# Kernel optimization log

Measured on AMD Instinct MI355X. Metric: run time of the kernel, lower is better.

## Reference

```python
import jax, jax.numpy as jnp
import numpy as np

EMBED = 768
HEADS = 12
FFN = 3072
EPS = 1e-5

def _linear_params(key, din, dout):
    k1, k2 = jax.random.split(key)
    s = 1.0 / np.sqrt(din)
    W = jax.random.uniform(k1, (din, dout), minval=-s, maxval=s, dtype=jnp.float32)
    b = jax.random.uniform(k2, (dout,), minval=-s, maxval=s, dtype=jnp.float32)
    return W, b

def setup_inputs() -> dict:
    key = jax.random.key(0)
    ks = jax.random.split(key, 8)
    x = jax.random.normal(ks[0], (1, 4096, EMBED), dtype=jnp.float32)
    Wq, bq = _linear_params(ks[1], EMBED, EMBED)
    Wk, bk = _linear_params(ks[2], EMBED, EMBED)
    Wv, bv = _linear_params(ks[3], EMBED, EMBED)
    Wo, bo = _linear_params(ks[4], EMBED, EMBED)
    W1, b1 = _linear_params(ks[5], EMBED, FFN)
    W2, b2 = _linear_params(ks[6], FFN, EMBED)
    ln1_g = jnp.ones((EMBED,), jnp.float32); ln1_b = jnp.zeros((EMBED,), jnp.float32)
    ln2_g = jnp.ones((EMBED,), jnp.float32); ln2_b = jnp.zeros((EMBED,), jnp.float32)
    return {"x": x, "Wq": Wq, "bq": bq, "Wk": Wk, "bk": bk, "Wv": Wv, "bv": bv,
            "Wo": Wo, "bo": bo, "ln1_g": ln1_g, "ln1_b": ln1_b,
            "ln2_g": ln2_g, "ln2_b": ln2_b, "W1": W1, "b1": b1, "W2": W2, "b2": b2}

def _layernorm(x, g, b):
    mu = jnp.mean(x, axis=-1, keepdims=True)
    var = jnp.mean(jnp.square(x - mu), axis=-1, keepdims=True)
    return (x - mu) * jax.lax.rsqrt(var + EPS) * g + b

def _block(x, Wq, bq, Wk, bk, Wv, bv, Wo, bo, ln1_g, ln1_b, ln2_g, ln2_b, W1, b1, W2, b2):
    B, T, C = x.shape
    H = HEADS
    D = C // H
    # pre-LN
    h = _layernorm(x, ln1_g, ln1_b)
    # naive causal self-attention with explicit [B,H,T,T] scores (as in source)
    q = (h @ Wq + bq).reshape(B, T, H, D).transpose(0, 2, 1, 3)  # bhtd
    k = (h @ Wk + bk).reshape(B, T, H, D).transpose(0, 2, 1, 3)
    v = (h @ Wv + bv).reshape(B, T, H, D).transpose(0, 2, 1, 3)
    scores = jnp.einsum('bhqd,bhkd->bhqk', q, k) / jnp.sqrt(jnp.float32(D))
    causal = jnp.tril(jnp.ones((T, T), dtype=bool))  # True = keep
    scores = jnp.where(causal, scores, -jnp.inf)
    attn = jax.nn.softmax(scores, axis=-1)
    ctx = jnp.einsum('bhqk,bhkd->bhqd', attn, v)
    ctx = ctx.transpose(0, 2, 1, 3).reshape(B, T, C)
    y = ctx @ Wo + bo
    x = y + h  # residual onto ln1 output (source adds to post-LN x)
    # second LN + MLP
    h2 = _layernorm(x, ln2_g, ln2_b)
    m = jax.nn.gelu(h2 @ W1 + b1, approximate=False) @ W2 + b2
    return m + h2

def reference(x, Wq, bq, Wk, bk, Wv, bv, Wo, bo, ln1_g, ln1_b, ln2_g, ln2_b, W1, b1, W2, b2):
    return _block(x, Wq, bq, Wk, bk, Wv, bv, Wo, bo, ln1_g, ln1_b, ln2_g, ln2_b, W1, b1, W2, b2)
```

## Files before the change

### kernel.cpp

```cpp
#include <hip/hip_runtime.h>
#include <math.h>

#define EMBED 768
#define FFN_D 3072
#define TSEQ 4096
#define NHEAD 12
#define DHEAD 64
#define CQKV 2304
#define NSPLIT 4
#define NQITEMS 192
#define SC2Q 0.180336880111120419f

typedef _Float16 f16;
typedef __attribute__((ext_vector_type(2))) _Float16 f16x2;
typedef __attribute__((ext_vector_type(4))) _Float16 f16x4;
typedef __attribute__((ext_vector_type(8))) _Float16 f16x8;
typedef __attribute__((ext_vector_type(4))) float f32x4;

#if __has_builtin(__builtin_amdgcn_exp2f)
#define EXP2(x) __builtin_amdgcn_exp2f(x)
#else
#define EXP2(x) exp2f(x)
#endif

__device__ __forceinline__ f16x2 pkrtz(float a, float b) {
    return __builtin_bit_cast(f16x2, __builtin_amdgcn_cvt_pkrtz(a, b));
}

__device__ __forceinline__ void gload16(const f16* g, f16* lds) {
    __builtin_amdgcn_global_load_lds((const __attribute__((address_space(1))) void*)g,
                                     (__attribute__((address_space(3))) void*)lds, 16, 0, 0);
}

__global__ __launch_bounds__(256) void prep_kernel(const float* __restrict__ Wq,
                                                   const float* __restrict__ Wk,
                                                   const float* __restrict__ Wv,
                                                   const float* __restrict__ Wo,
                                                   const float* __restrict__ W1,
                                                   const float* __restrict__ W2,
                                                   const float* __restrict__ bq,
                                                   const float* __restrict__ bk,
                                                   const float* __restrict__ bv,
                                                   f16* __restrict__ WqkvT,
                                                   f16* __restrict__ WoT,
                                                   f16* __restrict__ W1T,
                                                   f16* __restrict__ W2T,
                                                   float* __restrict__ bqkv) {
    const int b = blockIdx.x;
    const int t = threadIdx.x;
    if (b == 1728) {
#pragma unroll
        for (int i = 0; i < 9; i++) {
            int idx = i * 256 + t;
            if (idx < 768) bqkv[idx] = bq[idx];
            else if (idx < 1536) bqkv[idx] = bk[idx - 768];
            else if (idx < 2304) bqkv[idx] = bv[idx - 1536];
        }
        return;
    }
    const float* W; f16* WT; int din, dout, local;
    if (b < 144)       { W = Wq; WT = WqkvT;                 din = 768;  dout = 768;  local = b; }
    else if (b < 288)  { W = Wk; WT = WqkvT + 768 * 768;     din = 768;  dout = 768;  local = b - 144; }
    else if (b < 432)  { W = Wv; WT = WqkvT + 2 * 768 * 768; din = 768;  dout = 768;  local = b - 288; }
    else if (b < 576)  { W = Wo; WT = WoT;                   din = 768;  dout = 768;  local = b - 432; }
    else if (b < 1152) { W = W1; WT = W1T;                   din = 768;  dout = 3072; local = b - 576; }
    else               { W = W2; WT = W2T;                   din = 3072; dout = 768;  local = b - 1152; }
    const int ntx = dout / 64;
    const int j0 = (local % ntx) * 64;
    const int i0 = (local / ntx) * 64;
    __shared__ float tile[64][65];
    const int tx = t & 63;
    const int ty = t >> 6;
#pragma unroll
    for (int rr = ty; rr < 64; rr += 4)
        tile[rr][tx] = W[(size_t)(i0 + rr) * dout + j0 + tx];
    __syncthreads();
    const int half = t & 31;
    const int rw = t >> 5;
#pragma unroll
    for (int rr = rw; rr < 64; rr += 8) {
        f16x2 v = {(f16)tile[2 * half][rr], (f16)tile[2 * half + 1][rr]};
        *(f16x2*)&WT[(size_t)(j0 + rr) * din + i0 + 2 * half] = v;
    }
}

__global__ __launch_bounds__(256) void ln_kernel(const float* __restrict__ x,
                                                 const float* __restrict__ g,
                                                 const float* __restrict__ b,
                                                 f16* __restrict__ hh) {
    const int row = blockIdx.x;
    const float* xr = x + (size_t)row * EMBED;
    const int t = threadIdx.x;
    float v0 = xr[t], v1 = xr[t + 256], v2 = xr[t + 512];
    float s = v0 + v1 + v2;
#pragma unroll
    for (int m = 1; m < 64; m <<= 1) s += __shfl_xor(s, m);
    __shared__ float red[4], red2[4];
    const int wid = t >> 6, lane = t & 63;
    if (lane == 0) red[wid] = s;
    __syncthreads();
    float mean = (red[0] + red[1] + red[2] + red[3]) * (1.0f / 768.0f);
    float d0 = v0 - mean, d1 = v1 - mean, d2 = v2 - mean;
    float ss = d0 * d0 + d1 * d1 + d2 * d2;
#pragma unroll
    for (int m = 1; m < 64; m <<= 1) ss += __shfl_xor(ss, m);
    if (lane == 0) red2[wid] = ss;
    __syncthreads();
    float inv = rsqrtf((red2[0] + red2[1] + red2[2] + red2[3]) * (1.0f / 768.0f) + 1e-5f);
    size_t base = (size_t)row * EMBED;
    hh[base + t]       = (f16)(d0 * inv * g[t] + b[t]);
    hh[base + t + 256] = (f16)(d1 * inv * g[t + 256] + b[t + 256]);
    hh[base + t + 512] = (f16)(d2 * inv * g[t + 512] + b[t + 512]);
}

template <int EPI, int BM, int BN>
__global__ __launch_bounds__(256) void gemm_kernel(const f16* __restrict__ A,
                                                   const f16* __restrict__ BT,
                                                   const float* __restrict__ bias,
                                                   const f16* __restrict__ resh,
                                                   float* __restrict__ outf,
                                                   f16* __restrict__ outh,
                                                   f16* __restrict__ vtout,
                                                   int M, int N, int K) {
    constexpr int IM = BM / 32;
    constexpr int JN = BN / 32;
    __shared__ __align__(16) f16 As[BM][64];
    __shared__ __align__(16) f16 Bs[BN][64];
    const int t = threadIdx.x;
    const int nbx = gridDim.x;
    const int nwg = nbx * gridDim.y;
    int bid = blockIdx.x + blockIdx.y * nbx;
    bid = (bid & 7) * (nwg >> 3) + (bid >> 3);
    const int m0 = (bid / nbx) * BM;
    const int n0 = (bid % nbx) * BN;
    const int wid = t >> 6;
    const int lane = t & 63;
    const int wm = (wid >> 1) * (BM / 2);
    const int wn = (wid & 1) * (BN / 2);
    const int lr = lane & 15;
    const int quad = lane >> 4;
    const int sr = lane >> 3;
    const int scn = (lane & 7) ^ sr;
    const int xv = lr & 7;

    f32x4 zero = {0.f, 0.f, 0.f, 0.f};
    f32x4 acc[IM][JN];
#pragma unroll
    for (int i = 0; i < IM; i++)
#pragma unroll
        for (int j = 0; j < JN; j++) acc[i][j] = zero;

    const f16* Ap = A + (size_t)(m0 + wid * (BM / 4) + sr) * K + scn * 8;
    const f16* Bp = BT + (size_t)(n0 + wid * (BN / 4) + sr) * K + scn * 8;

    for (int k0 = 0; k0 < K; k0 += 64) {
        __syncthreads();
#pragma unroll
        for (int c = 0; c < BM / 32; c++)
            gload16(Ap + (size_t)(c * 8) * K + k0, &As[wid * (BM / 4) + c * 8][0]);
#pragma unroll
        for (int c = 0; c < BN / 32; c++)
            gload16(Bp + (size_t)(c * 8) * K + k0, &Bs[wid * (BN / 4) + c * 8][0]);
        __syncthreads();
#pragma unroll
        for (int ks = 0; ks < 2; ks++) {
            f16x8 af[IM], bf[JN];
#pragma unroll
            for (int i = 0; i < IM; i++)
                af[i] = *(const f16x8*)&As[wm + i * 16 + lr][((ks * 4 + quad) ^ xv) * 8];
#pragma unroll
            for (int j = 0; j < JN; j++)
                bf[j] = *(const f16x8*)&Bs[wn + j * 16 + lr][((ks * 4 + quad) ^ xv) * 8];
#pragma unroll
            for (int i = 0; i < IM; i++)
#pragma unroll
                for (int j = 0; j < JN; j++)
                    acc[i][j] = __builtin_amdgcn_mfma_f32_16x16x32_f16(bf[j], af[i], acc[i][j], 0, 0, 0);
        }
    }

    const bool vsec = (EPI == 0) && (n0 >= 2 * EMBED);
#pragma unroll
    for (int i = 0; i < IM; i++) {
        const int row = m0 + wm + i * 16 + lr;
#pragma unroll
        for (int j = 0; j < JN; j++) {
            const int col = n0 + wn + j * 16 + quad * 4;
            const float4 bv = *(const float4*)&bias[col];
            float v0 = acc[i][j][0] + bv.x;
            float v1 = acc[i][j][1] + bv.y;
            float v2 = acc[i][j][2] + bv.z;
            float v3 = acc[i][j][3] + bv.w;
            const size_t idx = (size_t)row * N + col;
            if (EPI == 0) {
                if (vsec) {
                    const int c0 = col - 2 * EMBED;
                    vtout[(size_t)(c0 + 0) * TSEQ + row] = (f16)v0;
                    vtout[(size_t)(c0 + 1) * TSEQ + row] = (f16)v1;
                    vtout[(size_t)(c0 + 2) * TSEQ + row] = (f16)v2;
                    vtout[(size_t)(c0 + 3) * TSEQ + row] = (f16)v3;
                } else {
                    const float qs = (col < EMBED) ? SC2Q : 1.0f;
                    f16x4 hv = {(f16)(v0 * qs), (f16)(v1 * qs), (f16)(v2 * qs), (f16)(v3 * qs)};
                    *(f16x4*)&outh[idx] = hv;
                }
            } else if (EPI == 1) {
                const f16x4 rr = *(const f16x4*)&resh[idx];
                f32x4 ov = {v0 + (float)rr[0], v1 + (float)rr[1], v2 + (float)rr[2], v3 + (float)rr[3]};
                *(f32x4*)&outf[idx] = ov;
            } else {
                f16x4 hv = {(f16)(0.5f * v0 * (1.0f + erff(v0 * 0.70710678118654752f))),
                            (f16)(0.5f * v1 * (1.0f + erff(v1 * 0.70710678118654752f))),
                            (f16)(0.5f * v2 * (1.0f + erff(v2 * 0.70710678118654752f))),
                            (f16)(0.5f * v3 * (1.0f + erff(v3 * 0.70710678118654752f)))};
                *(f16x4*)&outh[idx] = hv;
            }
        }
    }
}

__global__ __launch_bounds__(256) void attn_kernel(const f16* __restrict__ qkv,
                                                   const f16* __restrict__ vT,
                                                   f16* __restrict__ OpartH,
                                                   float2* __restrict__ ml,
                                                   int* __restrict__ ctr) {
    __shared__ __align__(16) f16 Ks[64][72];
    __shared__ __align__(16) f16 Vt[64][72];
    __shared__ int s_item;
    const int t = threadIdx.x;
    const int wid = t >> 6;
    const int lane = t & 63;
    const int lr = lane & 15;
    const int quad = lane >> 4;
    const int srow = t >> 3;
    const int scol = (t & 7) * 8;
    const int pA = (t & 1) * 16 + ((t >> 1) & 1) * 4 + (t & 4) * 8;
    const int xq = blockIdx.x & 7;

    for (;;) {
        __syncthreads();
        if (t == 0) s_item = atomicAdd(&ctr[xq], 1);
        __syncthreads();
        const int item = s_item;
        if (item >= NQITEMS) return;
        const int qb = 31 - item / 6;
        const int u = xq * 6 + item % 6;
        const int h = u >> 2;
        const int sp = u & 3;
        const int q0 = qb * 128;

        const int nkb = 2 * qb + 2;
        const int chunk = (nkb + NSPLIT - 1) / NSPLIT;
        const int kb0 = sp * chunk;
        const int kb1 = min(nkb, kb0 + chunk);
        const int wrow0 = q0 + wid * 32;

        float m_i[2] = {-INFINITY, -INFINITY};
        float l_lane[2] = {0.f, 0.f};
        f32x4 zero = {0.f, 0.f, 0.f, 0.f};
        f32x4 o[4][2];
#pragma unroll
        for (int dt = 0; dt < 4; dt++)
#pragma unroll
            for (int qt = 0; qt < 2; qt++) o[dt][qt] = zero;

        f16x8 qf[2][2];
        int4 kreg[2], vreg[2];
        const f16* kbase = qkv + EMBED + (size_t)h * DHEAD;
        const f16* vbase = vT + (size_t)h * DHEAD * TSEQ;
        if (kb0 < kb1) {
#pragma unroll
            for (int qt = 0; qt < 2; qt++)
#pragma unroll
                for (int dh = 0; dh < 2; dh++)
                    qf[qt][dh] = *(const f16x8*)(qkv + (size_t)(wrow0 + qt * 16 + lr) * CQKV
                                                 + h * DHEAD + dh * 32 + quad * 8);
            const int k0 = kb0 * 64;
#pragma unroll
            for (int p = 0; p < 2; p++) {
                kreg[p] = *(const int4*)(kbase + (size_t)(k0 + p * 32 + srow) * CQKV + scol);
                vreg[p] = *(const int4*)(vbase + (size_t)(p * 32 + srow) * TSEQ + k0 + scol);
            }
        }

        for (int kb = kb0; kb < kb1; ++kb) {
            const int k0 = kb * 64;
            __syncthreads();
#pragma unroll
            for (int p = 0; p < 2; p++) {
                *(int4*)&Ks[p * 32 + srow][scol] = kreg[p];
                *(int2*)&Vt[p * 32 + srow][pA]     = make_int2(vreg[p].x, vreg[p].y);
                *(int2*)&Vt[p * 32 + srow][pA + 8] = make_int2(vreg[p].z, vreg[p].w);
            }
            __syncthreads();
            if (kb + 1 < kb1) {
                const int kn = (kb + 1) * 64;
#pragma unroll
                for (int p = 0; p < 2; p++) {
                    kreg[p] = *(const int4*)(kbase + (size_t)(kn + p * 32 + srow) * CQKV + scol);
                    vreg[p] = *(const int4*)(vbase + (size_t)(p * 32 + srow) * TSEQ + kn + scol);
                }
            }

            if (k0 <= wrow0 + 31) {
                f32x4 s[4][2];
#pragma unroll
                for (int kt = 0; kt < 4; kt++)
#pragma unroll
                    for (int qt = 0; qt < 2; qt++) s[kt][qt] = zero;
#pragma unroll
                for (int dh = 0; dh < 2; dh++) {
#pragma unroll
                    for (int kt = 0; kt < 4; kt++) {
                        f16x8 kf = *(const f16x8*)&Ks[kt * 16 + lr][dh * 32 + quad * 8];
#pragma unroll
                        for (int qt = 0; qt < 2; qt++)
                            s[kt][qt] = __builtin_amdgcn_mfma_f32_16x16x32_f16(kf, qf[qt][dh], s[kt][qt], 0, 0, 0);
                    }
                }
                if (k0 + 63 > wrow0) {
#pragma unroll
                    for (int kt = 0; kt < 4; kt++)
#pragma unroll
                        for (int qt = 0; qt < 2; qt++)
#pragma unroll
                            for (int r = 0; r < 4; r++) {
                                int key = k0 + kt * 16 + quad * 4 + r;
                                int row = wrow0 + qt * 16 + lr;
                                if (key > row) s[kt][qt][r] = -INFINITY;
                            }
                }
                float mx[2];
#pragma unroll
                for (int qt = 0; qt < 2; qt++) {
                    float a[4];
#pragma unroll
                    for (int kt = 0; kt < 4; kt++)
                        a[kt] = fmaxf(fmaxf(s[kt][qt][0], s[kt][qt][1]),
                                      fmaxf(s[kt][qt][2], s[kt][qt][3]));
                    float m = fmaxf(fmaxf(a[0], a[1]), fmaxf(a[2], a[3]));
                    m = fmaxf(m, __shfl_xor(m, 16));
                    m = fmaxf(m, __shfl_xor(m, 32));
                    mx[qt] = m;
                }
                if (__any((mx[0] > m_i[0] + 4.f) || (mx[1] > m_i[1] + 4.f))) {
#pragma unroll
                    for (int qt = 0; qt < 2; qt++) {
                        float mn = fmaxf(m_i[qt], mx[qt]);
                        float al = EXP2(m_i[qt] - mn);
                        m_i[qt] = mn;
                        l_lane[qt] *= al;
#pragma unroll
                        for (int dt = 0; dt < 4; dt++)
#pragma unroll
                            for (int r = 0; r < 4; r++) o[dt][qt][r] *= al;
                    }
                }
                union PW { f16x8 v8; f16x2 h2[4]; };
                PW pw[2][2];
                float rs[2] = {0.f, 0.f};
#pragma unroll
                for (int kt = 0; kt < 4; kt++)
#pragma unroll
                    for (int qt = 0; qt < 2; qt++) {
                        float p0 = EXP2(s[kt][qt][0] - m_i[qt]);
                        float p1 = EXP2(s[kt][qt][1] - m_i[qt]);
                        float p2 = EXP2(s[kt][qt][2] - m_i[qt]);
                        float p3 = EXP2(s[kt][qt][3] - m_i[qt]);
                        rs[qt] += (p0 + p1) + (p2 + p3);
                        pw[kt >> 1][qt].h2[(kt & 1) * 2]     = pkrtz(p0, p1);
                        pw[kt >> 1][qt].h2[(kt & 1) * 2 + 1] = pkrtz(p2, p3);
                    }
#pragma unroll
                for (int qt = 0; qt < 2; qt++) l_lane[qt] += rs[qt];
#pragma unroll
                for (int s2 = 0; s2 < 2; s2++)
#pragma unroll
                    for (int dt = 0; dt < 4; dt++) {
                        f16x8 vf = *(const f16x8*)&Vt[dt * 16 + lr][s2 * 32 + quad * 8];
#pragma unroll
                        for (int qt = 0; qt < 2; qt++)
                            o[dt][qt] = __builtin_amdgcn_mfma_f32_16x16x32_f16(vf, pw[s2][qt].v8, o[dt][qt], 0, 0, 0);
                    }
            }
        }

        float l_i[2];
#pragma unroll
        for (int qt = 0; qt < 2; qt++) {
            float v2 = l_lane[qt];
            v2 += __shfl_xor(v2, 16);
            v2 += __shfl_xor(v2, 32);
            l_i[qt] = v2;
        }
        __syncthreads();
        f16* ob = ((wid & 2) ? &Vt[0][0] : &Ks[0][0]) + (wid & 1) * (32 * 72);
#pragma unroll
        for (int qt = 0; qt < 2; qt++)
#pragma unroll
            for (int dt = 0; dt < 4; dt++) {
                f16x4 oh = {(f16)o[dt][qt][0], (f16)o[dt][qt][1], (f16)o[dt][qt][2], (f16)o[dt][qt][3]};
                *(f16x4*)&ob[(qt * 16 + lr) * 72 + dt * 16 + quad * 4] = oh;
            }
        const int rl = lane >> 3;
        const int ck = lane & 7;
#pragma unroll
        for (int i = 0; i < 4; i++) {
            const int row_l = rl + i * 8;
            f16x8 val = *(const f16x8*)&ob[row_l * 72 + ck * 8];
            *(f16x8*)&OpartH[((size_t)sp * TSEQ + wrow0 + row_l) * EMBED + h * DHEAD + ck * 8] = val;
        }
#pragma unroll
        for (int qt = 0; qt < 2; qt++)
            if (quad == 0) {
                int row = wrow0 + qt * 16 + lr;
                ml[((size_t)sp * TSEQ + row) * NHEAD + h] = make_float2(m_i[qt], l_i[qt]);
            }
    }
}

__global__ __launch_bounds__(128) void attn_merge_kernel(const f16* __restrict__ OpartH,
                                                         const float2* __restrict__ ml,
                                                         f16* __restrict__ ctx) {
    const int row = blockIdx.x;
    const int t = threadIdx.x;
    __shared__ float wgt[NSPLIT][NHEAD];
    if (t < NHEAD) {
        float m[NSPLIT], l[NSPLIT];
        float M = -INFINITY;
#pragma unroll
        for (int s = 0; s < NSPLIT; s++) {
            float2 v = ml[((size_t)s * TSEQ + row) * NHEAD + t];
            m[s] = v.x; l[s] = v.y;
            M = fmaxf(M, m[s]);
        }
        float L = 0.f;
        float w[NSPLIT];
#pragma unroll
        for (int s = 0; s < NSPLIT; s++) {
            w[s] = exp2f(m[s] - M);
            L += l[s] * w[s];
        }
        float rL = 1.0f / L;
#pragma unroll
        for (int s = 0; s < NSPLIT; s++) wgt[s][t] = w[s] * rL;
    }
    __syncthreads();
    if (t < 96) {
        const int h = t >> 3;
        float acc[8] = {0.f, 0.f, 0.f, 0.f, 0.f, 0.f, 0.f, 0.f};
#pragma unroll
        for (int s = 0; s < NSPLIT; s++) {
            const float w = wgt[s][h];
            f16x8 v = *(const f16x8*)&OpartH[((size_t)s * TSEQ + row) * EMBED + t * 8];
#pragma unroll
            for (int e = 0; e < 8; e++) acc[e] += w * (float)v[e];
        }
        f16x8 out;
#pragma unroll
        for (int e = 0; e < 8; e++) out[e] = (f16)acc[e];
        *(f16x8*)&ctx[(size_t)row * EMBED + t * 8] = out;
    }
}

extern "C" void kernel_launch(void* const* d_in, const int* in_sizes, int n_in,
                              void* d_out, int out_size, void* d_ws, size_t ws_size,
                              hipStream_t stream) {
    const float* x     = (const float*)d_in[0];
    const float* Wq    = (const float*)d_in[1];
    const float* bq    = (const float*)d_in[2];
    const float* Wk    = (const float*)d_in[3];
    const float* bk    = (const float*)d_in[4];
    const float* Wv    = (const float*)d_in[5];
    const float* bv    = (const float*)d_in[6];
    const float* Wo    = (const float*)d_in[7];
    const float* bo    = (const float*)d_in[8];
    const float* ln1_g = (const float*)d_in[9];
    const float* ln1_b = (const float*)d_in[10];
    const float* ln2_g = (const float*)d_in[11];
    const float* ln2_b = (const float*)d_in[12];
    const float* W1    = (const float*)d_in[13];
    const float* b1    = (const float*)d_in[14];
    const float* W2    = (const float*)d_in[15];
    const float* b2    = (const float*)d_in[16];

    char* p = (char*)d_ws;
    auto alloc = [&](size_t bytes) -> void* {
        void* r = (void*)p;
        p += (bytes + 255) & ~(size_t)255;
        return r;
    };
    f16*   WqkvT = (f16*)alloc((size_t)CQKV * EMBED * 2);
    f16*   WoT   = (f16*)alloc((size_t)EMBED * EMBED * 2);
    f16*   W1T   = (f16*)alloc((size_t)FFN_D * EMBED * 2);
    f16*   W2T   = (f16*)alloc((size_t)EMBED * FFN_D * 2);
    float* bqkv  = (float*)alloc((size_t)CQKV * 4);
    f16*   hh    = (f16*)alloc((size_t)TSEQ * EMBED * 2);
    f16*   qkv   = (f16*)alloc((size_t)TSEQ * CQKV * 2);
    f16*   vT    = (f16*)alloc((size_t)EMBED * TSEQ * 2);
    f16*   ctx   = (f16*)alloc((size_t)TSEQ * EMBED * 2);
    float* x2    = (float*)alloc((size_t)TSEQ * EMBED * 4);
    f16*   h2h   = (f16*)alloc((size_t)TSEQ * EMBED * 2);
    f16*   m1    = (f16*)alloc((size_t)TSEQ * FFN_D * 2);
    int*   ctr   = (int*)alloc(256);

    f16*    OpartH = m1;
    float2* mlbuf  = (float2*)x2;

    dim3 blk(256);
    prep_kernel<<<dim3(1729), blk, 0, stream>>>(Wq, Wk, Wv, Wo, W1, W2, bq, bk, bv,
                                                WqkvT, WoT, W1T, W2T, bqkv);
    ln_kernel<<<dim3(TSEQ), blk, 0, stream>>>(x, ln1_g, ln1_b, hh);
    gemm_kernel<0, 64, 128><<<dim3(CQKV / 128, TSEQ / 64), blk, 0, stream>>>(
        hh, WqkvT, bqkv, nullptr, nullptr, qkv, vT, TSEQ, CQKV, EMBED);
    (void)hipMemsetAsync(ctr, 0, 256, stream);
    attn_kernel<<<dim3(768), blk, 0, stream>>>(qkv, vT, OpartH, mlbuf, ctr);
    attn_merge_kernel<<<dim3(TSEQ), dim3(128), 0, stream>>>(OpartH, mlbuf, ctx);
    gemm_kernel<1, 64, 64><<<dim3(EMBED / 64, TSEQ / 64), blk, 0, stream>>>(
        ctx, WoT, bo, hh, x2, nullptr, nullptr, TSEQ, EMBED, EMBED);
    ln_kernel<<<dim3(TSEQ), blk, 0, stream>>>(x2, ln2_g, ln2_b, h2h);
    gemm_kernel<2, 128, 128><<<dim3(FFN_D / 128, TSEQ / 128), blk, 0, stream>>>(
        h2h, W1T, b1, nullptr, nullptr, m1, nullptr, TSEQ, FFN_D, EMBED);
    gemm_kernel<1, 64, 64><<<dim3(EMBED / 64, TSEQ / 64), blk, 0, stream>>>(
        m1, W2T, b2, h2h, (float*)d_out, nullptr, nullptr, TSEQ, EMBED, FFN_D);
}
```

Baseline: 318.6 us.

## Double-buffer GEMM LDS tiles, batch merge rows, shrink FFN1 tile

The GEMM main loop now keeps two LDS buffers and issues the next K-tile's global-to-LDS copy before computing on the current one, dropping one barrier per iteration. The attention merge kernel handles four rows per block, with each thread computing its own split weights instead of going through shared memory and a barrier. The FFN1 GEMM moves from 128x128 to 64x128 tiles for more workgroups. Double buffering doubles LDS use, and its correctness depends on gload16 completing before the loop-end barrier.

```diff
diff --git a/kernel.cpp b/kernel.cpp
--- a/kernel.cpp
+++ b/kernel.cpp
@@ -124,8 +124,8 @@
                                                    int M, int N, int K) {
     constexpr int IM = BM / 32;
     constexpr int JN = BN / 32;
-    __shared__ __align__(16) f16 As[BM][64];
-    __shared__ __align__(16) f16 Bs[BN][64];
+    __shared__ __align__(16) f16 As[2][BM][64];
+    __shared__ __align__(16) f16 Bs[2][BN][64];
     const int t = threadIdx.x;
     const int nbx = gridDim.x;
     const int nwg = nbx * gridDim.y;
@@ -153,30 +153,37 @@
     const f16* Ap = A + (size_t)(m0 + wid * (BM / 4) + sr) * K + scn * 8;
     const f16* Bp = BT + (size_t)(n0 + wid * (BN / 4) + sr) * K + scn * 8;
 
+    auto stage = [&](int buf, int k0) {
+#pragma unroll
+        for (int c = 0; c < BM / 32; c++)
+            gload16(Ap + (size_t)(c * 8) * K + k0, &As[buf][wid * (BM / 4) + c * 8][0]);
+#pragma unroll
+        for (int c = 0; c < BN / 32; c++)
+            gload16(Bp + (size_t)(c * 8) * K + k0, &Bs[buf][wid * (BN / 4) + c * 8][0]);
+    };
+
+    stage(0, 0);
+    __syncthreads();
+    int cur = 0;
     for (int k0 = 0; k0 < K; k0 += 64) {
-        __syncthreads();
-#pragma unroll
-        for (int c = 0; c < BM / 32; c++)
-            gload16(Ap + (size_t)(c * 8) * K + k0, &As[wid * (BM / 4) + c * 8][0]);
-#pragma unroll
-        for (int c = 0; c < BN / 32; c++)
-            gload16(Bp + (size_t)(c * 8) * K + k0, &Bs[wid * (BN / 4) + c * 8][0]);
-        __syncthreads();
+        if (k0 + 64 < K) stage(cur ^ 1, k0 + 64);
 #pragma unroll
         for (int ks = 0; ks < 2; ks++) {
             f16x8 af[IM], bf[JN];
 #pragma unroll
             for (int i = 0; i < IM; i++)
-                af[i] = *(const f16x8*)&As[wm + i * 16 + lr][((ks * 4 + quad) ^ xv) * 8];
+                af[i] = *(const f16x8*)&As[cur][wm + i * 16 + lr][((ks * 4 + quad) ^ xv) * 8];
 #pragma unroll
             for (int j = 0; j < JN; j++)
-                bf[j] = *(const f16x8*)&Bs[wn + j * 16 + lr][((ks * 4 + quad) ^ xv) * 8];
+                bf[j] = *(const f16x8*)&Bs[cur][wn + j * 16 + lr][((ks * 4 + quad) ^ xv) * 8];
 #pragma unroll
             for (int i = 0; i < IM; i++)
 #pragma unroll
                 for (int j = 0; j < JN; j++)
                     acc[i][j] = __builtin_amdgcn_mfma_f32_16x16x32_f16(bf[j], af[i], acc[i][j], 0, 0, 0);
         }
+        __syncthreads();
+        cur ^= 1;
     }
 
     const bool vsec = (EPI == 0) && (n0 >= 2 * EMBED);
@@ -422,15 +429,17 @@
 __global__ __launch_bounds__(128) void attn_merge_kernel(const f16* __restrict__ OpartH,
                                                          const float2* __restrict__ ml,
                                                          f16* __restrict__ ctx) {
-    const int row = blockIdx.x;
     const int t = threadIdx.x;
-    __shared__ float wgt[NSPLIT][NHEAD];
-    if (t < NHEAD) {
+    if (t >= 96) return;
+    const int h = t >> 3;
+#pragma unroll
+    for (int r = 0; r < 4; r++) {
+        const int row = blockIdx.x * 4 + r;
         float m[NSPLIT], l[NSPLIT];
         float M = -INFINITY;
 #pragma unroll
         for (int s = 0; s < NSPLIT; s++) {
-            float2 v = ml[((size_t)s * TSEQ + row) * NHEAD + t];
+            float2 v = ml[((size_t)s * TSEQ + row) * NHEAD + h];
             m[s] = v.x; l[s] = v.y;
             M = fmaxf(M, m[s]);
         }
@@ -441,20 +450,14 @@
             w[s] = exp2f(m[s] - M);
             L += l[s] * w[s];
         }
-        float rL = 1.0f / L;
-#pragma unroll
-        for (int s = 0; s < NSPLIT; s++) wgt[s][t] = w[s] * rL;
-    }
-    __syncthreads();
-    if (t < 96) {
-        const int h = t >> 3;
+        const float rL = 1.0f / L;
         float acc[8] = {0.f, 0.f, 0.f, 0.f, 0.f, 0.f, 0.f, 0.f};
 #pragma unroll
         for (int s = 0; s < NSPLIT; s++) {
-            const float w = wgt[s][h];
+            const float ws = w[s] * rL;
             f16x8 v = *(const f16x8*)&OpartH[((size_t)s * TSEQ + row) * EMBED + t * 8];
 #pragma unroll
-            for (int e = 0; e < 8; e++) acc[e] += w * (float)v[e];
+            for (int e = 0; e < 8; e++) acc[e] += ws * (float)v[e];
         }
         f16x8 out;
 #pragma unroll
@@ -515,11 +518,11 @@
         hh, WqkvT, bqkv, nullptr, nullptr, qkv, vT, TSEQ, CQKV, EMBED);
     (void)hipMemsetAsync(ctr, 0, 256, stream);
     attn_kernel<<<dim3(768), blk, 0, stream>>>(qkv, vT, OpartH, mlbuf, ctr);
-    attn_merge_kernel<<<dim3(TSEQ), dim3(128), 0, stream>>>(OpartH, mlbuf, ctx);
+    attn_merge_kernel<<<dim3(TSEQ / 4), dim3(128), 0, stream>>>(OpartH, mlbuf, ctx);
     gemm_kernel<1, 64, 64><<<dim3(EMBED / 64, TSEQ / 64), blk, 0, stream>>>(
         ctx, WoT, bo, hh, x2, nullptr, nullptr, TSEQ, EMBED, EMBED);
     ln_kernel<<<dim3(TSEQ), blk, 0, stream>>>(x2, ln2_g, ln2_b, h2h);
-    gemm_kernel<2, 128, 128><<<dim3(FFN_D / 128, TSEQ / 128), blk, 0, stream>>>(
+    gemm_kernel<2, 64, 128><<<dim3(FFN_D / 128, TSEQ / 64), blk, 0, stream>>>(
         h2h, W1T, b1, nullptr, nullptr, m1, nullptr, TSEQ, FFN_D, EMBED);
     gemm_kernel<1, 64, 64><<<dim3(EMBED / 64, TSEQ / 64), blk, 0, stream>>>(
         m1, W2T, b2, h2h, (float*)d_out, nullptr, nullptr, TSEQ, EMBED, FFN_D);
```

Measured after the change: 327.7 us. +2.8%, slower.
